# Optimization experiments

Hardware: AMD Instinct MI355X
Metric: run time of the kernel (lower is better)

Reference implementation:

```python
import jax, jax.numpy as jnp
import numpy as np

B, T, C = 8, 4096, 1024


def setup_inputs() -> dict:
    key = jax.random.key(0)
    ks = jax.random.split(key, 5)
    scales = (jnp.arange(C, dtype=jnp.float32) / C).reshape(1, 1, C)
    return {
        "x": jax.random.normal(ks[0], (B, T, C), dtype=jnp.float32),
        "time_decay": scales,
        "time_first": scales,
        "time_mix_k": scales,
        "time_mix_v": scales,
        "time_mix_r": scales,
        "Wk": jax.random.normal(ks[1], (C, C), dtype=jnp.float32) / np.sqrt(C),
        "Wv": jax.random.normal(ks[2], (C, C), dtype=jnp.float32) / np.sqrt(C),
        "Wr": jax.random.normal(ks[3], (C, C), dtype=jnp.float32) / np.sqrt(C),
        "Wo": jax.random.normal(ks[4], (C, C), dtype=jnp.float32) / np.sqrt(C),
    }


def _wkv(w_decay, u_first, k, v):
    # w_decay, u_first: [C]; k, v: [B, T, C]
    w = -jnp.exp(w_decay)  # per original: w = -w.exp()
    u = u_first
    kt = jnp.transpose(k, (1, 0, 2))  # [T, B, C]
    vt = jnp.transpose(v, (1, 0, 2))
    a0 = jnp.zeros((k.shape[0], k.shape[2]), dtype=k.dtype)
    b0 = jnp.zeros_like(a0)
    p0 = jnp.full_like(a0, -1e38)  # running max exponent

    def step(carry, kv):
        a, b, p = carry
        k_t, v_t = kv
        # output at t (includes bonus u for current token)
        q = jnp.maximum(p, u + k_t)
        e1 = jnp.exp(p - q)
        e2 = jnp.exp(u + k_t - q)
        y = (e1 * a + e2 * v_t) / (e1 * b + e2)
        # state update with decay w
        q2 = jnp.maximum(p + w, k_t)
        f1 = jnp.exp(p + w - q2)
        f2 = jnp.exp(k_t - q2)
        return (f1 * a + f2 * v_t, f1 * b + f2, q2), y

    _, y = jax.lax.scan(step, (a0, b0, p0), (kt, vt))
    return jnp.transpose(y, (1, 0, 2))  # [B, T, C]


def reference(x, time_decay, time_first, time_mix_k, time_mix_v, time_mix_r, Wk, Wv, Wr, Wo):
    # time shift: prev token, zero-padded at t=0 (ZeroPad2d((0,0,1,-1)))
    x_prev = jnp.pad(x, ((0, 0), (1, 0), (0, 0)))[:, :-1]
    # torch.lerp(a, b, w) = a + w*(b-a)
    xk = x_prev + time_mix_k * (x - x_prev)
    xv = x_prev + time_mix_v * (x - x_prev)
    xr = x_prev + time_mix_r * (x - x_prev)
    k = jnp.einsum('btc,dc->btd', xk, Wk)
    v = jnp.einsum('btc,dc->btd', xv, Wv)
    sr = jax.nn.sigmoid(jnp.einsum('btc,dc->btd', xr, Wr))
    wkv = _wkv(time_decay.reshape(-1), time_first.reshape(-1), k, v)
    return jnp.einsum('btc,dc->btd', sr * wkv, Wo)
```

## Files before the change

kernel.cpp:

```cpp
#include <hip/hip_runtime.h>
#include <hip/hip_bf16.h>
#include <hip/hip_fp16.h>


#define BH 8
#define TT 4096
#define CC 1024
#define NCH 64
#define CHL (TT / NCH)

typedef _Float16       f16x8  __attribute__((ext_vector_type(8)));
typedef float          f32x4  __attribute__((ext_vector_type(4)));
typedef unsigned short ushort_t;

__device__ __forceinline__ ushort_t f2h_u(float f) {
  return __half_as_ushort(__float2half(f));
}

#define GLOAD_LDS16(g, l)                                                     \
  __builtin_amdgcn_global_load_lds(                                           \
      (const __attribute__((address_space(1))) unsigned int*)(g),             \
      (__attribute__((address_space(3))) unsigned int*)(l), 16, 0, 0)

#define BARRIER() do { asm volatile("" ::: "memory");                        \
                       __builtin_amdgcn_s_barrier();                          \
                       asm volatile("" ::: "memory"); } while (0)

#define LGKM0() do { asm volatile("s_waitcnt lgkmcnt(0)" ::: "memory");      \
                     __builtin_amdgcn_sched_barrier(0); } while (0)

#define WAITV(n) do { asm volatile("s_waitcnt vmcnt(" #n ")" ::: "memory");  \
                      __builtin_amdgcn_sched_barrier(0); } while (0)

__global__ __launch_bounds__(256)
void split_w(const float* __restrict__ W0, const float* __restrict__ W1,
             const float* __restrict__ W2, const float* __restrict__ W3,
             ushort_t* __restrict__ out)
{
  int idx = blockIdx.x * 256 + threadIdx.x;
  int w = idx >> 20;
  int e = idx & (CC * CC - 1);
  const float* src = (w == 0) ? W0 : (w == 1) ? W1 : (w == 2) ? W2 : W3;
  out[(size_t)w * CC * CC + e] = f2h_u(src[e]);
}

__global__ __launch_bounds__(256)
void lerp3(const float* __restrict__ x,
           const float* __restrict__ mk, const float* __restrict__ mv,
           const float* __restrict__ mr,
           ushort_t* __restrict__ xk, ushort_t* __restrict__ xv,
           ushort_t* __restrict__ xr)
{
  const int idx = blockIdx.x * 256 + threadIdx.x;
  const int m = idx >> 8;
  const int c = (idx & 255) * 4;
  const size_t e = (size_t)m * CC + c;
  float4 cu = *(const float4*)(x + e);
  float4 pv = make_float4(0.f, 0.f, 0.f, 0.f);
  if ((m & (TT - 1)) != 0) pv = *(const float4*)(x + e - CC);

  const float* mixes[3] = {mk, mv, mr};
  ushort_t* outs[3] = {xk, xv, xr};
  #pragma unroll
  for (int z = 0; z < 3; ++z) {
    float4 mx = *(const float4*)(mixes[z] + c);
    float a0 = pv.x + mx.x * (cu.x - pv.x);
    float a1 = pv.y + mx.y * (cu.y - pv.y);
    float a2 = pv.z + mx.z * (cu.z - pv.z);
    float a3 = pv.w + mx.w * (cu.w - pv.w);
    *(ushort4*)(outs[z] + e) = make_ushort4(f2h_u(a0), f2h_u(a1), f2h_u(a2), f2h_u(a3));
  }
}

template<int EPI>
__global__ __launch_bounds__(512)
void gemm_f16(const ushort_t* __restrict__ Ab, const ushort_t* __restrict__ Bb,
              void* __restrict__ Dv)
{
  constexpr int NS = 16;
  const size_t nbt = (size_t)BH * TT * CC;

  __shared__ __align__(16) ushort_t lds[2][2][2][8192];

  const int tid  = threadIdx.x;
  const int wave = tid >> 6, lane = tid & 63;
  const int wm = wave & 1, wn = wave >> 1;
  const int lr = lane & 15, kg = lane >> 4;

  const int z = blockIdx.z;
  const ushort_t* Ah = Ab + (size_t)z * nbt;
  const ushort_t* Bh = Bb + (size_t)z * CC * CC;

  const int bid = blockIdx.x;
  const int swz = (bid & 7) * 64 + (bid >> 3);
  const int m0 = (swz >> 2) * 256;
  const int n0 = (swz & 3) * 256;

  f32x4 acc[8][4] = {};

  auto stage = [&](int s, int h) {
    if (s >= NS) return;
    const int kk = s * 64 + h * 32;
    #pragma unroll
    for (int op = 0; op < 2; ++op) {
      const ushort_t* g0 = op ? Bh : Ah;
      const int r0 = op ? n0 : m0;
      #pragma unroll
      for (int c = 0; c < 2; ++c) {
        const int row = c * 128 + (tid >> 2);
        const int q   = (tid & 3) ^ ((row >> 1) & 3);
        const ushort_t* src = g0 + (size_t)(r0 + row) * CC + kk + q * 8;
        ushort_t* dst = &lds[s & 1][h][op][c * 4096 + wave * 512];
        GLOAD_LDS16(src, dst);
      }
    }
  };
  auto rdA = [&](int b, int h, int fm) -> f16x8 {
    const int row = wm * 128 + fm * 16 + lr;
    const int q   = kg ^ ((row >> 1) & 3);
    return *(const f16x8*)&lds[b][h][0][row * 32 + q * 8];
  };
  auto rdB = [&](int b, int h, int fn) -> f16x8 {
    const int row = wn * 64 + fn * 16 + lr;
    const int q   = kg ^ ((row >> 1) & 3);
    return *(const f16x8*)&lds[b][h][1][row * 32 + q * 8];
  };

  stage(0, 0); stage(0, 1); stage(1, 0); stage(1, 1);
  WAITV(8);
  BARRIER();

  f16x8 Acur[8];
  #pragma unroll
  for (int fm = 0; fm < 8; ++fm) Acur[fm] = rdA(0, 0, fm);

  for (int s = 0; s < NS; ++s) {
    const int b = s & 1;

    f16x8 Bfr[4];
    #pragma unroll
    for (int fn = 0; fn < 4; ++fn) Bfr[fn] = rdB(b, 0, fn);
    f16x8 Anx[8];
    #pragma unroll
    for (int fm = 0; fm < 8; ++fm) Anx[fm] = rdA(b, 1, fm);
    __builtin_amdgcn_s_setprio(1);
    #pragma unroll
    for (int fm = 0; fm < 8; ++fm)
      #pragma unroll
      for (int fn = 0; fn < 4; ++fn)
        acc[fm][fn] = __builtin_amdgcn_mfma_f32_16x16x32_f16(Acur[fm], Bfr[fn], acc[fm][fn], 0, 0, 0);
    __builtin_amdgcn_s_setprio(0);
    LGKM0();
    BARRIER();
    stage(s + 2, 0);
    if (s == NS - 2) { WAITV(4); } else { WAITV(8); }

    f16x8 Bf2[4];
    #pragma unroll
    for (int fn = 0; fn < 4; ++fn) Bf2[fn] = rdB(b, 1, fn);
    #pragma unroll
    for (int fm = 0; fm < 8; ++fm) Acur[fm] = rdA(b ^ 1, 0, fm);
    __builtin_amdgcn_s_setprio(1);
    #pragma unroll
    for (int fm = 0; fm < 8; ++fm)
      #pragma unroll
      for (int fn = 0; fn < 4; ++fn)
        acc[fm][fn] = __builtin_amdgcn_mfma_f32_16x16x32_f16(Anx[fm], Bf2[fn], acc[fm][fn], 0, 0, 0);
    __builtin_amdgcn_s_setprio(0);
    LGKM0();
    BARRIER();
    stage(s + 2, 1);
    if (s == NS - 2)      { WAITV(0); }
    else if (s < NS - 2)  { WAITV(8); }
  }

  if (EPI == 0) {
    float* Df = (float*)Dv;
    #pragma unroll
    for (int fm = 0; fm < 8; ++fm)
      #pragma unroll
      for (int fn = 0; fn < 4; ++fn) {
        const int col  = n0 + wn * 64 + fn * 16 + lr;
        const int rowb = m0 + wm * 128 + fm * 16 + kg * 4;
        #pragma unroll
        for (int r = 0; r < 4; ++r)
          Df[(size_t)(rowb + r) * CC + col] = acc[fm][fn][r];
      }
  } else {
    __half* Dh = (__half*)Dv + (size_t)z * nbt;
    __half* ep = (__half*)&lds[0][0][0][0];
    const int rowl = tid >> 4;
    const int ck   = tid & 15;
    #pragma unroll
    for (int s = 0; s < 8; ++s) {
      __syncthreads();
      #pragma unroll
      for (int fn = 0; fn < 4; ++fn)
        #pragma unroll
        for (int r = 0; r < 4; ++r)
          ep[(wm * 16 + kg * 4 + r) * 256 + wn * 64 + fn * 16 + lr] =
              __float2half(acc[s][fn][r]);
      __syncthreads();
      uint4 v0 = *(const uint4*)&ep[rowl * 256 + ck * 16];
      uint4 v1 = *(const uint4*)&ep[rowl * 256 + ck * 16 + 8];
      const int grow = m0 + (rowl >> 4) * 128 + s * 16 + (rowl & 15);
      __half* dst = Dh + (size_t)grow * CC + n0 + ck * 16;
      *(uint4*)dst = v0;
      *(uint4*)(dst + 8) = v1;
    }
  }
}

__global__ __launch_bounds__(256)
void wkv_phase_a(const __half* __restrict__ kb, const __half* __restrict__ vb,
                 const float* __restrict__ decay,
                 float* __restrict__ SA, float* __restrict__ SB, float* __restrict__ SP)
{
  const int idx = blockIdx.x * 256 + threadIdx.x;
  const int c  = idx & (CC - 1);
  const int bc = idx >> 10;
  const int ch = bc & (NCH - 1);
  const int b  = bc >> 6;
  const float w = -__expf(decay[c]);
  float aa = 0.f, bb = 0.f, pp = -1e38f;
  size_t base = ((size_t)b * TT + (size_t)ch * CHL) * CC + c;
  #pragma unroll 4
  for (int t = 0; t < CHL; ++t) {
    const float kt = __half2float(kb[base]);
    const float vt = __half2float(vb[base]);
    const float q2 = fmaxf(pp + w, kt);
    const float f1 = __expf(pp + w - q2);
    const float f2 = __expf(kt - q2);
    aa = f1 * aa + f2 * vt; bb = f1 * bb + f2; pp = q2;
    base += CC;
  }
  SA[idx] = aa; SB[idx] = bb; SP[idx] = pp;
}

__global__ __launch_bounds__(256)
void wkv_combine(float* __restrict__ SA, float* __restrict__ SB, float* __restrict__ SP,
                 const float* __restrict__ decay)
{
  const int idx = blockIdx.x * 256 + threadIdx.x;
  const int c = idx & (CC - 1);
  const int b = idx >> 10;
  const float w  = -__expf(decay[c]);
  const float wL = w * (float)CHL;
  float aa = 0.f, bb = 0.f, pp = -1e38f;
  for (int ch = 0; ch < NCH; ++ch) {
    const size_t s = ((size_t)b * NCH + ch) * CC + c;
    const float la = SA[s], lb = SB[s], lp = SP[s];
    SA[s] = aa; SB[s] = bb; SP[s] = pp;
    const float pw = pp + wL;
    const float q  = fmaxf(pw, lp);
    const float e1 = __expf(pw - q);
    const float e2 = __expf(lp - q);
    aa = e1 * aa + e2 * la; bb = e1 * bb + e2 * lb; pp = q;
  }
}

__global__ __launch_bounds__(256)
void wkv_phase_c(const __half* __restrict__ kb, const __half* __restrict__ vb,
                 const __half* __restrict__ rb, const float* __restrict__ decay,
                 const float* __restrict__ first,
                 const float* __restrict__ SA, const float* __restrict__ SB,
                 const float* __restrict__ SP,
                 ushort_t* __restrict__ yh)
{
  const int idx = blockIdx.x * 256 + threadIdx.x;
  const int c  = idx & (CC - 1);
  const int bc = idx >> 10;
  const int ch = bc & (NCH - 1);
  const int b  = bc >> 6;
  const float w = -__expf(decay[c]);
  const float u = first[c];
  float aa = SA[idx], bb = SB[idx], pp = SP[idx];
  size_t base = ((size_t)b * TT + (size_t)ch * CHL) * CC + c;
  #pragma unroll 4
  for (int t = 0; t < CHL; ++t) {
    const float kt = __half2float(kb[base]);
    const float vt = __half2float(vb[base]);
    const float rt = __half2float(rb[base]);
    const float q  = fmaxf(pp, u + kt);
    const float e1 = __expf(pp - q);
    const float e2 = __expf(u + kt - q);
    const float yv = (e1 * aa + e2 * vt) / (e1 * bb + e2);
    const float sr = 1.f / (1.f + __expf(-rt));
    yh[base] = f2h_u(sr * yv);
    const float q2 = fmaxf(pp + w, kt);
    const float f1 = __expf(pp + w - q2);
    const float f2 = __expf(kt - q2);
    aa = f1 * aa + f2 * vt; bb = f1 * bb + f2; pp = q2;
    base += CC;
  }
}

extern "C" void kernel_launch(void* const* d_in, const int* in_sizes, int n_in,
                              void* d_out, int out_size, void* d_ws, size_t ws_size,
                              hipStream_t stream) {
  const float* x     = (const float*)d_in[0];
  const float* decay = (const float*)d_in[1];
  const float* first = (const float*)d_in[2];
  const float* mk    = (const float*)d_in[3];
  const float* mv    = (const float*)d_in[4];
  const float* mr    = (const float*)d_in[5];
  const float* Wk    = (const float*)d_in[6];
  const float* Wv    = (const float*)d_in[7];
  const float* Wr    = (const float*)d_in[8];
  const float* Wo    = (const float*)d_in[9];
  float* out = (float*)d_out;

  const size_t nbt = (size_t)BH * TT * CC;
  const size_t WS  = (size_t)CC * CC;
  char* p = (char*)d_ws;
  ushort_t* xk   = (ushort_t*)(p);
  ushort_t* xv   = (ushort_t*)(p +  67108864);
  ushort_t* xr   = (ushort_t*)(p + 134217728);
  __half*   kbuf = (__half*)  (p + 201326592);
  __half*   vbuf = (__half*)  (p + 268435456);
  __half*   rbuf = (__half*)  (p + 335544320);
  ushort_t* Wsp  = (ushort_t*)(p + 402653184);
  float*    SA   = (float*)   (p + 411041792);
  float*    SB   = (float*)   (p + 413138944);
  float*    SP   = (float*)   (p + 415236096);

  dim3 blk(256);
  const dim3 gblk(512);
  const unsigned lerpg = (unsigned)(nbt / 4 / 256);

  split_w<<<dim3(4 * CC * CC / 256), blk, 0, stream>>>(Wk, Wv, Wr, Wo, Wsp);
  lerp3<<<dim3(lerpg), blk, 0, stream>>>(x, mk, mv, mr, xk, xv, xr);

  gemm_f16<1><<<dim3(512, 1, 3), gblk, 0, stream>>>(xk, Wsp, (void*)kbuf);

  const int nscan = BH * NCH * CC;
  wkv_phase_a<<<dim3(nscan / 256), blk, 0, stream>>>(kbuf, vbuf, decay, SA, SB, SP);
  wkv_combine<<<dim3(BH * CC / 256), blk, 0, stream>>>(SA, SB, SP, decay);
  wkv_phase_c<<<dim3(nscan / 256), blk, 0, stream>>>(kbuf, vbuf, rbuf, decay, first,
                                                     SA, SB, SP, xk);

  gemm_f16<0><<<dim3(512, 1, 1), gblk, 0, stream>>>(xk, Wsp + 3 * WS, (void*)out);
}
```

Measured before the change: 499.6 us.

## Shrink GEMM tile to 128x256 with K32 stages to raise occupancy

The f16 MFMA GEMM tile shrinks from 256x256 to 128x256, and each pipeline stage now covers K=32 instead of two 32-wide halves, which cuts LDS use to 48KB per block. The grid doubles to 1024 blocks and launch bounds request 4 waves per SIMD, so more blocks can be resident. The register-prefetch pipelining of A fragments is dropped in favour of a simpler loop that waits on both vector and LDS counters before each barrier. This trades per-block data reuse and overlap for higher occupancy. The epilogue LDS stride is padded to 280 to reduce bank conflicts.

```diff
diff --git a/kernel.cpp b/kernel.cpp
--- a/kernel.cpp
+++ b/kernel.cpp
@@ -26,8 +26,8 @@
                        __builtin_amdgcn_s_barrier();                          \
                        asm volatile("" ::: "memory"); } while (0)
 
-#define LGKM0() do { asm volatile("s_waitcnt lgkmcnt(0)" ::: "memory");      \
-                     __builtin_amdgcn_sched_barrier(0); } while (0)
+#define WAITALL() do { asm volatile("s_waitcnt vmcnt(0) lgkmcnt(0)" ::: "memory"); \
+                       __builtin_amdgcn_sched_barrier(0); } while (0)
 
 #define WAITV(n) do { asm volatile("s_waitcnt vmcnt(" #n ")" ::: "memory");  \
                       __builtin_amdgcn_sched_barrier(0); } while (0)
@@ -73,14 +73,14 @@
 }
 
 template<int EPI>
-__global__ __launch_bounds__(512)
+__global__ __launch_bounds__(512, 4)
 void gemm_f16(const ushort_t* __restrict__ Ab, const ushort_t* __restrict__ Bb,
               void* __restrict__ Dv)
 {
-  constexpr int NS = 16;
+  constexpr int NS = 32;
   const size_t nbt = (size_t)BH * TT * CC;
 
-  __shared__ __align__(16) ushort_t lds[2][2][2][8192];
+  __shared__ __align__(16) ushort_t lds[2][12288];
 
   const int tid  = threadIdx.x;
   const int wave = tid >> 6, lane = tid & 63;
@@ -92,118 +92,99 @@
   const ushort_t* Bh = Bb + (size_t)z * CC * CC;
 
   const int bid = blockIdx.x;
-  const int swz = (bid & 7) * 64 + (bid >> 3);
-  const int m0 = (swz >> 2) * 256;
+  const int swz = (bid & 7) * 128 + (bid >> 3);
+  const int m0 = (swz >> 2) * 128;
   const int n0 = (swz & 3) * 256;
 
-  f32x4 acc[8][4] = {};
-
-  auto stage = [&](int s, int h) {
+  f32x4 acc[4][4] = {};
+
+  auto stage = [&](int s) {
     if (s >= NS) return;
-    const int kk = s * 64 + h * 32;
-    #pragma unroll
-    for (int op = 0; op < 2; ++op) {
-      const ushort_t* g0 = op ? Bh : Ah;
-      const int r0 = op ? n0 : m0;
-      #pragma unroll
-      for (int c = 0; c < 2; ++c) {
-        const int row = c * 128 + (tid >> 2);
-        const int q   = (tid & 3) ^ ((row >> 1) & 3);
-        const ushort_t* src = g0 + (size_t)(r0 + row) * CC + kk + q * 8;
-        ushort_t* dst = &lds[s & 1][h][op][c * 4096 + wave * 512];
-        GLOAD_LDS16(src, dst);
-      }
+    const int kk = s * 32;
+    {
+      const int row = tid >> 2;
+      const int q   = (tid & 3) ^ ((row >> 1) & 3);
+      const ushort_t* src = Ah + (size_t)(m0 + row) * CC + kk + q * 8;
+      ushort_t* dst = &lds[s & 1][0] + wave * 512;
+      GLOAD_LDS16(src, dst);
+    }
+    #pragma unroll
+    for (int c = 0; c < 2; ++c) {
+      const int row = c * 128 + (tid >> 2);
+      const int q   = (tid & 3) ^ ((row >> 1) & 3);
+      const ushort_t* src = Bh + (size_t)(n0 + row) * CC + kk + q * 8;
+      ushort_t* dst = &lds[s & 1][4096] + c * 4096 + wave * 512;
+      GLOAD_LDS16(src, dst);
     }
   };
-  auto rdA = [&](int b, int h, int fm) -> f16x8 {
-    const int row = wm * 128 + fm * 16 + lr;
+  auto rdA = [&](int b, int fm) -> f16x8 {
+    const int row = wm * 64 + fm * 16 + lr;
     const int q   = kg ^ ((row >> 1) & 3);
-    return *(const f16x8*)&lds[b][h][0][row * 32 + q * 8];
+    return *(const f16x8*)&lds[b][row * 32 + q * 8];
   };
-  auto rdB = [&](int b, int h, int fn) -> f16x8 {
+  auto rdB = [&](int b, int fn) -> f16x8 {
     const int row = wn * 64 + fn * 16 + lr;
     const int q   = kg ^ ((row >> 1) & 3);
-    return *(const f16x8*)&lds[b][h][1][row * 32 + q * 8];
+    return *(const f16x8*)&lds[b][4096 + row * 32 + q * 8];
   };
 
-  stage(0, 0); stage(0, 1); stage(1, 0); stage(1, 1);
-  WAITV(8);
+  stage(0); stage(1);
+  WAITV(3);
   BARRIER();
-
-  f16x8 Acur[8];
-  #pragma unroll
-  for (int fm = 0; fm < 8; ++fm) Acur[fm] = rdA(0, 0, fm);
 
   for (int s = 0; s < NS; ++s) {
     const int b = s & 1;
 
     f16x8 Bfr[4];
     #pragma unroll
-    for (int fn = 0; fn < 4; ++fn) Bfr[fn] = rdB(b, 0, fn);
-    f16x8 Anx[8];
-    #pragma unroll
-    for (int fm = 0; fm < 8; ++fm) Anx[fm] = rdA(b, 1, fm);
+    for (int fn = 0; fn < 4; ++fn) Bfr[fn] = rdB(b, fn);
+    f16x8 Afr[4];
+    #pragma unroll
+    for (int fm = 0; fm < 4; ++fm) Afr[fm] = rdA(b, fm);
+
     __builtin_amdgcn_s_setprio(1);
     #pragma unroll
-    for (int fm = 0; fm < 8; ++fm)
+    for (int fm = 0; fm < 4; ++fm)
       #pragma unroll
       for (int fn = 0; fn < 4; ++fn)
-        acc[fm][fn] = __builtin_amdgcn_mfma_f32_16x16x32_f16(Acur[fm], Bfr[fn], acc[fm][fn], 0, 0, 0);
+        acc[fm][fn] = __builtin_amdgcn_mfma_f32_16x16x32_f16(Afr[fm], Bfr[fn], acc[fm][fn], 0, 0, 0);
     __builtin_amdgcn_s_setprio(0);
-    LGKM0();
+
+    WAITALL();
     BARRIER();
-    stage(s + 2, 0);
-    if (s == NS - 2) { WAITV(4); } else { WAITV(8); }
-
-    f16x8 Bf2[4];
-    #pragma unroll
-    for (int fn = 0; fn < 4; ++fn) Bf2[fn] = rdB(b, 1, fn);
-    #pragma unroll
-    for (int fm = 0; fm < 8; ++fm) Acur[fm] = rdA(b ^ 1, 0, fm);
-    __builtin_amdgcn_s_setprio(1);
-    #pragma unroll
-    for (int fm = 0; fm < 8; ++fm)
-      #pragma unroll
-      for (int fn = 0; fn < 4; ++fn)
-        acc[fm][fn] = __builtin_amdgcn_mfma_f32_16x16x32_f16(Anx[fm], Bf2[fn], acc[fm][fn], 0, 0, 0);
-    __builtin_amdgcn_s_setprio(0);
-    LGKM0();
-    BARRIER();
-    stage(s + 2, 1);
-    if (s == NS - 2)      { WAITV(0); }
-    else if (s < NS - 2)  { WAITV(8); }
+    stage(s + 2);
   }
 
   if (EPI == 0) {
     float* Df = (float*)Dv;
     #pragma unroll
-    for (int fm = 0; fm < 8; ++fm)
+    for (int fm = 0; fm < 4; ++fm)
       #pragma unroll
       for (int fn = 0; fn < 4; ++fn) {
         const int col  = n0 + wn * 64 + fn * 16 + lr;
-        const int rowb = m0 + wm * 128 + fm * 16 + kg * 4;
+        const int rowb = m0 + wm * 64 + fm * 16 + kg * 4;
         #pragma unroll
         for (int r = 0; r < 4; ++r)
           Df[(size_t)(rowb + r) * CC + col] = acc[fm][fn][r];
       }
   } else {
     __half* Dh = (__half*)Dv + (size_t)z * nbt;
-    __half* ep = (__half*)&lds[0][0][0][0];
+    __half* ep = (__half*)&lds[0][0];
     const int rowl = tid >> 4;
     const int ck   = tid & 15;
     #pragma unroll
-    for (int s = 0; s < 8; ++s) {
+    for (int s = 0; s < 4; ++s) {
       __syncthreads();
       #pragma unroll
       for (int fn = 0; fn < 4; ++fn)
         #pragma unroll
         for (int r = 0; r < 4; ++r)
-          ep[(wm * 16 + kg * 4 + r) * 256 + wn * 64 + fn * 16 + lr] =
+          ep[(wm * 16 + kg * 4 + r) * 280 + wn * 64 + fn * 16 + lr] =
               __float2half(acc[s][fn][r]);
       __syncthreads();
-      uint4 v0 = *(const uint4*)&ep[rowl * 256 + ck * 16];
-      uint4 v1 = *(const uint4*)&ep[rowl * 256 + ck * 16 + 8];
-      const int grow = m0 + (rowl >> 4) * 128 + s * 16 + (rowl & 15);
+      uint4 v0 = *(const uint4*)&ep[rowl * 280 + ck * 16];
+      uint4 v1 = *(const uint4*)&ep[rowl * 280 + ck * 16 + 8];
+      const int grow = m0 + (rowl >> 4) * 64 + s * 16 + (rowl & 15);
       __half* dst = Dh + (size_t)grow * CC + n0 + ck * 16;
       *(uint4*)dst = v0;
       *(uint4*)(dst + 8) = v1;
@@ -331,7 +312,7 @@
   split_w<<<dim3(4 * CC * CC / 256), blk, 0, stream>>>(Wk, Wv, Wr, Wo, Wsp);
   lerp3<<<dim3(lerpg), blk, 0, stream>>>(x, mk, mv, mr, xk, xv, xr);
 
-  gemm_f16<1><<<dim3(512, 1, 3), gblk, 0, stream>>>(xk, Wsp, (void*)kbuf);
+  gemm_f16<1><<<dim3(1024, 1, 3), gblk, 0, stream>>>(xk, Wsp, (void*)kbuf);
 
   const int nscan = BH * NCH * CC;
   wkv_phase_a<<<dim3(nscan / 256), blk, 0, stream>>>(kbuf, vbuf, decay, SA, SB, SP);
@@ -339,5 +320,5 @@
   wkv_phase_c<<<dim3(nscan / 256), blk, 0, stream>>>(kbuf, vbuf, rbuf, decay, first,
                                                      SA, SB, SP, xk);
 
-  gemm_f16<0><<<dim3(512, 1, 1), gblk, 0, stream>>>(xk, Wsp + 3 * WS, (void*)out);
-}
+  gemm_f16<0><<<dim3(1024, 1, 1), gblk, 0, stream>>>(xk, Wsp + 3 * WS, (void*)out);
+}
```

Result: slower. 517.4 us (+3.6%).

## Restructure GEMM main loop into quarter-step MFMA phases for two-block occupancy

Applied to the files above, without the earlier changes.

The f16 GEMM main loop is split into four phases per k-step. Each phase holds only 4 A fragments instead of 8 and issues one global-to-LDS load part at a time, with finer-grained barriers. This lowers register pressure so the kernel can target two 512-thread blocks per CU, which the new launch bounds request. The epilogue LDS staging stride is padded from 256 to 280 to reduce bank conflicts. In exchange the kernel takes more barriers per step and gives up the register-held prefetch of the next A fragments.

```diff
diff --git a/kernel.cpp b/kernel.cpp
--- a/kernel.cpp
+++ b/kernel.cpp
@@ -73,14 +73,14 @@
 }
 
 template<int EPI>
-__global__ __launch_bounds__(512)
+__global__ __launch_bounds__(512, 2)
 void gemm_f16(const ushort_t* __restrict__ Ab, const ushort_t* __restrict__ Bb,
               void* __restrict__ Dv)
 {
   constexpr int NS = 16;
   const size_t nbt = (size_t)BH * TT * CC;
 
-  __shared__ __align__(16) ushort_t lds[2][2][2][8192];
+  __shared__ __align__(16) ushort_t lds[2][4][8192];
 
   const int tid  = threadIdx.x;
   const int wave = tid >> 6, lane = tid & 63;
@@ -98,80 +98,102 @@
 
   f32x4 acc[8][4] = {};
 
-  auto stage = [&](int s, int h) {
+  auto stage = [&](int s, int part) {
     if (s >= NS) return;
-    const int kk = s * 64 + h * 32;
-    #pragma unroll
-    for (int op = 0; op < 2; ++op) {
-      const ushort_t* g0 = op ? Bh : Ah;
-      const int r0 = op ? n0 : m0;
-      #pragma unroll
-      for (int c = 0; c < 2; ++c) {
-        const int row = c * 128 + (tid >> 2);
-        const int q   = (tid & 3) ^ ((row >> 1) & 3);
-        const ushort_t* src = g0 + (size_t)(r0 + row) * CC + kk + q * 8;
-        ushort_t* dst = &lds[s & 1][h][op][c * 4096 + wave * 512];
-        GLOAD_LDS16(src, dst);
-      }
+    const int kk = s * 64 + (part >> 1) * 32;
+    const ushort_t* g0 = (part & 1) ? Bh : Ah;
+    const int r0 = (part & 1) ? n0 : m0;
+    #pragma unroll
+    for (int c = 0; c < 2; ++c) {
+      const int row = c * 128 + (tid >> 2);
+      const int q   = (tid & 3) ^ ((row >> 1) & 3);
+      const ushort_t* src = g0 + (size_t)(r0 + row) * CC + kk + q * 8;
+      ushort_t* dst = &lds[s & 1][part][c * 4096 + wave * 512];
+      GLOAD_LDS16(src, dst);
     }
   };
-  auto rdA = [&](int b, int h, int fm) -> f16x8 {
+  auto rdA = [&](int b, int ks, int fm) -> f16x8 {
     const int row = wm * 128 + fm * 16 + lr;
     const int q   = kg ^ ((row >> 1) & 3);
-    return *(const f16x8*)&lds[b][h][0][row * 32 + q * 8];
+    return *(const f16x8*)&lds[b][ks * 2][row * 32 + q * 8];
   };
-  auto rdB = [&](int b, int h, int fn) -> f16x8 {
+  auto rdB = [&](int b, int ks, int fn) -> f16x8 {
     const int row = wn * 64 + fn * 16 + lr;
     const int q   = kg ^ ((row >> 1) & 3);
-    return *(const f16x8*)&lds[b][h][1][row * 32 + q * 8];
+    return *(const f16x8*)&lds[b][ks * 2 + 1][row * 32 + q * 8];
   };
 
-  stage(0, 0); stage(0, 1); stage(1, 0); stage(1, 1);
+  stage(0, 0); stage(0, 1); stage(0, 2); stage(0, 3);
+  stage(1, 0); stage(1, 1);
   WAITV(8);
   BARRIER();
 
-  f16x8 Acur[8];
-  #pragma unroll
-  for (int fm = 0; fm < 8; ++fm) Acur[fm] = rdA(0, 0, fm);
-
   for (int s = 0; s < NS; ++s) {
     const int b = s & 1;
-
-    f16x8 Bfr[4];
-    #pragma unroll
-    for (int fn = 0; fn < 4; ++fn) Bfr[fn] = rdB(b, 0, fn);
-    f16x8 Anx[8];
-    #pragma unroll
-    for (int fm = 0; fm < 8; ++fm) Anx[fm] = rdA(b, 1, fm);
+    f16x8 bfr[4], afr[4];
+
+    #pragma unroll
+    for (int fn = 0; fn < 4; ++fn) bfr[fn] = rdB(b, 0, fn);
+    #pragma unroll
+    for (int i = 0; i < 4; ++i) afr[i] = rdA(b, 0, i);
+    stage(s + 1, 2);
+    BARRIER();
+    LGKM0();
     __builtin_amdgcn_s_setprio(1);
     #pragma unroll
-    for (int fm = 0; fm < 8; ++fm)
-      #pragma unroll
-      for (int fn = 0; fn < 4; ++fn)
-        acc[fm][fn] = __builtin_amdgcn_mfma_f32_16x16x32_f16(Acur[fm], Bfr[fn], acc[fm][fn], 0, 0, 0);
+    for (int i = 0; i < 4; ++i)
+      #pragma unroll
+      for (int fn = 0; fn < 4; ++fn)
+        acc[i][fn] = __builtin_amdgcn_mfma_f32_16x16x32_f16(afr[i], bfr[fn], acc[i][fn], 0, 0, 0);
     __builtin_amdgcn_s_setprio(0);
+    BARRIER();
+
+    #pragma unroll
+    for (int i = 0; i < 4; ++i) afr[i] = rdA(b, 0, 4 + i);
+    stage(s + 1, 3);
+    BARRIER();
     LGKM0();
-    BARRIER();
+    __builtin_amdgcn_s_setprio(1);
+    #pragma unroll
+    for (int i = 0; i < 4; ++i)
+      #pragma unroll
+      for (int fn = 0; fn < 4; ++fn)
+        acc[4 + i][fn] = __builtin_amdgcn_mfma_f32_16x16x32_f16(afr[i], bfr[fn], acc[4 + i][fn], 0, 0, 0);
+    __builtin_amdgcn_s_setprio(0);
+    if (s < NS - 1) { WAITV(8); } else { WAITV(0); }
+    BARRIER();
+
+    #pragma unroll
+    for (int fn = 0; fn < 4; ++fn) bfr[fn] = rdB(b, 1, fn);
+    #pragma unroll
+    for (int i = 0; i < 4; ++i) afr[i] = rdA(b, 1, i);
     stage(s + 2, 0);
-    if (s == NS - 2) { WAITV(4); } else { WAITV(8); }
-
-    f16x8 Bf2[4];
-    #pragma unroll
-    for (int fn = 0; fn < 4; ++fn) Bf2[fn] = rdB(b, 1, fn);
-    #pragma unroll
-    for (int fm = 0; fm < 8; ++fm) Acur[fm] = rdA(b ^ 1, 0, fm);
+    BARRIER();
+    LGKM0();
     __builtin_amdgcn_s_setprio(1);
     #pragma unroll
-    for (int fm = 0; fm < 8; ++fm)
-      #pragma unroll
-      for (int fn = 0; fn < 4; ++fn)
-        acc[fm][fn] = __builtin_amdgcn_mfma_f32_16x16x32_f16(Anx[fm], Bf2[fn], acc[fm][fn], 0, 0, 0);
+    for (int i = 0; i < 4; ++i)
+      #pragma unroll
+      for (int fn = 0; fn < 4; ++fn)
+        acc[i][fn] = __builtin_amdgcn_mfma_f32_16x16x32_f16(afr[i], bfr[fn], acc[i][fn], 0, 0, 0);
     __builtin_amdgcn_s_setprio(0);
+    BARRIER();
+
+    #pragma unroll
+    for (int i = 0; i < 4; ++i) afr[i] = rdA(b, 1, 4 + i);
+    stage(s + 2, 1);
+    BARRIER();
     LGKM0();
-    BARRIER();
-    stage(s + 2, 1);
-    if (s == NS - 2)      { WAITV(0); }
-    else if (s < NS - 2)  { WAITV(8); }
+    __builtin_amdgcn_s_setprio(1);
+    #pragma unroll
+    for (int i = 0; i < 4; ++i)
+      #pragma unroll
+      for (int fn = 0; fn < 4; ++fn)
+        acc[4 + i][fn] = __builtin_amdgcn_mfma_f32_16x16x32_f16(afr[i], bfr[fn], acc[4 + i][fn], 0, 0, 0);
+    __builtin_amdgcn_s_setprio(0);
+    if (s < NS - 2)       { WAITV(8); }
+    else if (s == NS - 2) { WAITV(4); }
+    BARRIER();
   }
 
   if (EPI == 0) {
@@ -188,7 +210,7 @@
       }
   } else {
     __half* Dh = (__half*)Dv + (size_t)z * nbt;
-    __half* ep = (__half*)&lds[0][0][0][0];
+    __half* ep = (__half*)&lds[0][0][0];
     const int rowl = tid >> 4;
     const int ck   = tid & 15;
     #pragma unroll
@@ -198,11 +220,11 @@
       for (int fn = 0; fn < 4; ++fn)
         #pragma unroll
         for (int r = 0; r < 4; ++r)
-          ep[(wm * 16 + kg * 4 + r) * 256 + wn * 64 + fn * 16 + lr] =
+          ep[(wm * 16 + kg * 4 + r) * 280 + wn * 64 + fn * 16 + lr] =
               __float2half(acc[s][fn][r]);
       __syncthreads();
-      uint4 v0 = *(const uint4*)&ep[rowl * 256 + ck * 16];
-      uint4 v1 = *(const uint4*)&ep[rowl * 256 + ck * 16 + 8];
+      uint4 v0 = *(const uint4*)&ep[rowl * 280 + ck * 16];
+      uint4 v1 = *(const uint4*)&ep[rowl * 280 + ck * 16 + 8];
       const int grow = m0 + (rowl >> 4) * 128 + s * 16 + (rowl & 15);
       __half* dst = Dh + (size_t)grow * CC + n0 + ck * 16;
       *(uint4*)dst = v0;
```

Measured after the change: 492.6 us. About the same (-1.4%).
